# Optimization experiments

Hardware: AMD Instinct MI355X
Metric: run time of the kernel (lower is better)

Reference implementation:

```python
import jax, jax.numpy as jnp
import numpy as np

NMOL, NATOM, NPAIR = 32, 512, 32768
NBASIS, HIDDEN, NSPEC = 64, 256, 8
RC = 5.0
TOTNATOM = NMOL * NATOM


def setup_inputs() -> dict:
    key = jax.random.key(0)
    ks = jax.random.split(key, 8)
    cart = jax.random.normal(ks[0], (NMOL, NATOM, 3), jnp.float32) * 3.0
    shifts = jax.random.normal(ks[1], (NMOL, NPAIR, 3), jnp.float32) * 0.1
    species = jax.random.randint(ks[2], (NMOL, NATOM), 0, NSPEC)
    atom_index = jax.random.randint(ks[3], (2, NMOL, NPAIR), 0, NATOM)
    numatoms = jnp.full((NMOL,), NATOM, jnp.int32)
    centers = jnp.linspace(0.0, RC, NBASIS).astype(jnp.float32)
    widths = jnp.full((NBASIS,), 0.5, jnp.float32)
    c_emb = jax.random.normal(ks[4], (NSPEC, NBASIS), jnp.float32)
    W1 = jax.random.normal(ks[5], (NBASIS, HIDDEN), jnp.float32) / np.sqrt(NBASIS).astype(np.float32)
    b1 = jnp.zeros((HIDDEN,), jnp.float32)
    W2 = jax.random.normal(ks[6], (HIDDEN, 1), jnp.float32) / np.sqrt(HIDDEN).astype(np.float32)
    b2 = jnp.zeros((1,), jnp.float32)
    return dict(cart=cart, shifts=shifts, centers=centers, widths=widths, c_emb=c_emb,
                W1=W1, b1=b1, W2=W2, b2=b2,
                numatoms=numatoms, species=species, atom_index=atom_index)


def reference(cart, shifts, centers, widths, c_emb, W1, b1, W2, b2, numatoms, species, atom_index):
    species_flat = species.reshape(-1)                      # [totnatom]
    cart_flat = cart.reshape(-1, 3)                         # [totnatom, 3]
    # per-molecule atom offset, expanded over pairs (matches self_mol_index)
    mol_off = (jnp.arange(NMOL, dtype=atom_index.dtype) * NATOM)  # [nmol]
    off = jnp.broadcast_to(mol_off[:, None], (NMOL, NPAIR)).reshape(-1)  # [npairs_tot]
    idx12 = atom_index.reshape(2, -1) + off[None, :]        # [2, npairs_tot]
    shifts_flat = shifts.reshape(-1, 3)
    # padding mask (torch code drops rows with shift == -1e10; we mask instead)
    valid = jnp.all(shifts_flat > -1e10, axis=1)
    mask_f = valid.astype(cart.dtype)                       # [npairs_tot]
    # gather pair coords, periodic-shifted displacement
    c0 = cart_flat[idx12[0]]                                # [npairs_tot, 3]
    c1 = cart_flat[idx12[1]]
    dist_vec = (c0 - c1 + shifts_flat) * mask_f[:, None]    # [npairs_tot, 3]
    d = jnp.sqrt(jnp.sum(dist_vec * dist_vec, axis=1) + 1e-12)  # safe norm
    # embedded density: gaussian RBF * cosine cutoff * neighbor-species coeff
    rbf = jnp.exp(-widths[None, :] * (d[:, None] - centers[None, :]) ** 2)  # [P, nbasis]
    fc = 0.5 * (jnp.cos(jnp.pi * d / RC) + 1.0) * (d < RC).astype(cart.dtype)
    pair_feat = rbf * (fc * mask_f)[:, None] * c_emb[species_flat[idx12[1]]]
    density = jax.ops.segment_sum(pair_feat, idx12[0], num_segments=TOTNATOM)  # [totnatom, nbasis]
    # per-atom scalar output (nnmod)
    h = jax.nn.silu(density @ W1 + b1)
    output = (h @ W2 + b2).reshape(-1)                      # [totnatom]
    # scatter-add displacement vectors to center atom
    tot_vec = jax.ops.segment_sum(dist_vec, idx12[0], num_segments=TOTNATOM)  # [totnatom, 3]
    # weighted contraction ('i,ij->ij') + per-molecule sum -> dipole
    dipole = jnp.sum((output[:, None] * tot_vec).reshape(NMOL, NATOM, 3), axis=1)  # [nmol, 3]
    return dipole
```

## Files before the change

kernel.cpp:

```cpp
#include <hip/hip_runtime.h>

#define NMOL   32
#define NATOM  512
#define NPAIR  32768
#define NB     64
#define HIDDEN 256
#define TOTNATOM (NMOL * NATOM)
#define NSUB   8
#define BLKCAP4 4352
#define ABLK   4
#define NSLOT  128
#define CSLOT  64

typedef __attribute__((ext_vector_type(8))) short bf16x8;
typedef __attribute__((ext_vector_type(4))) float f32x4;

__device__ __forceinline__ unsigned short f2bf(float x) {
    unsigned u = __float_as_uint(x);
    u += 0x7FFFu + ((u >> 16) & 1u);
    return (unsigned short)(u >> 16);
}

__global__ __launch_bounds__(1024) void scatter_kernel(
    const float* __restrict__ cart, const float* __restrict__ shifts,
    const int* __restrict__ species, const int* __restrict__ atom_index,
    unsigned* __restrict__ cnt, unsigned* __restrict__ soff_g,
    float4* __restrict__ rec, float* __restrict__ dipole, int ndip)
{
    __shared__ float    s_cart[NATOM * 3];
    __shared__ int      s_sp[NATOM];
    __shared__ unsigned lcnt[NATOM];
    __shared__ unsigned pref[NATOM];
    __shared__ unsigned stot;
    __shared__ float4   list[BLKCAP4];

    const int tid  = threadIdx.x;
    const int lane = tid & 63;
    const int wave = tid >> 6;
    const int b    = blockIdx.x;
    const int mol  = b & 31;
    const int sub  = b >> 5;

    if (b == 0 && tid < ndip) dipole[tid] = 0.f;

    const float* cm = cart + (size_t)mol * NATOM * 3;
    const int*   sp = species + (size_t)mol * NATOM;
    for (int i = tid; i < NATOM * 3; i += 1024) s_cart[i] = cm[i];
    if (tid < NATOM) { lcnt[tid] = 0u; s_sp[tid] = sp[tid]; }
    __syncthreads();

    const int* ai0 = atom_index + (size_t)mol * NPAIR;
    const int* ai1 = ai0 + (size_t)NMOL * NPAIR;
    const float* sh = shifts + (size_t)mol * NPAIR * 3;
    const int base = sub * 4096;

    int   gi0[4], gi1[4];
    float gsx[4], gsy[4], gsz[4];
#pragma unroll
    for (int k = 0; k < 4; ++k) {
        const int p = base + k * 1024 + tid;
        gi0[k] = ai0[p];
        gi1[k] = ai1[p];
        gsx[k] = sh[p * 3 + 0];
        gsy[k] = sh[p * 3 + 1];
        gsz[k] = sh[p * 3 + 2];
    }

    float    rx[4], ry[4], rz[4];
    unsigned rs[4], rp[4];
    int      ri[4];
#pragma unroll
    for (int k = 0; k < 4; ++k) {
        const int a3 = gi0[k] * 3, b3 = gi1[k] * 3;
        const bool m = (gsx[k] > -1e10f && gsy[k] > -1e10f && gsz[k] > -1e10f);
        ri[k] = -1;
        if (m) {
            rx[k] = s_cart[a3 + 0] - s_cart[b3 + 0] + gsx[k];
            ry[k] = s_cart[a3 + 1] - s_cart[b3 + 1] + gsy[k];
            rz[k] = s_cart[a3 + 2] - s_cart[b3 + 2] + gsz[k];
            rs[k] = (unsigned)s_sp[gi1[k]];
            ri[k] = gi0[k];
            rp[k] = atomicAdd(&lcnt[gi0[k]], 1u);
        }
    }
    __syncthreads();

    if (wave == 0) {
        unsigned c[8], s = 0;
#pragma unroll
        for (int j = 0; j < 8; ++j) { c[j] = lcnt[lane * 8 + j]; s += c[j]; }
        unsigned incl = s;
#pragma unroll
        for (int off = 1; off < 64; off <<= 1) {
            const unsigned v = __shfl_up(incl, off);
            if (lane >= off) incl += v;
        }
        unsigned run = incl - s;
#pragma unroll
        for (int j = 0; j < 8; ++j) { pref[lane * 8 + j] = run; run += c[j]; }
        if (lane == 63) stot = incl;
    }
    __syncthreads();

#pragma unroll
    for (int k = 0; k < 4; ++k) {
        if (ri[k] >= 0) {
            const unsigned idx = pref[ri[k]] + rp[k];
            if (idx < (unsigned)BLKCAP4)
                list[idx] = make_float4(rx[k], ry[k], rz[k], __uint_as_float(rs[k]));
        }
    }
    __syncthreads();

    const int tot = min((int)stot, BLKCAP4);
    float4* dstr = rec + (size_t)b * BLKCAP4;
    for (int i = tid; i < tot; i += 1024) dstr[i] = list[i];

    if (tid < NATOM) {
        cnt[((size_t)mol * NATOM + tid) * NSUB + sub] = lcnt[tid];
        soff_g[(size_t)b * NATOM + tid] = pref[tid];
    }
}

__global__ __launch_bounds__(256) void gather_kernel(
    const unsigned* __restrict__ cnt, const unsigned* __restrict__ soff_g,
    const float4* __restrict__ rec,
    const float* __restrict__ centers, const float* __restrict__ widths,
    const float* __restrict__ c_emb,
    unsigned short* __restrict__ dens_bf, float* __restrict__ tvv)
{
    __shared__ float    cemb[8 * NB];
    __shared__ float4   list4[ABLK][NSLOT];
    __shared__ float2   cbuf[ABLK][CSLOT];
    __shared__ unsigned scnt[ABLK][NSUB];
    __shared__ unsigned sofg[ABLK][NSUB];
    __shared__ unsigned soff[ABLK][NSUB];
    __shared__ unsigned ntot[ABLK];

    const int tid   = threadIdx.x;
    const int B     = blockIdx.x;
    const int mol   = B & 31;
    const int inner = B >> 5;
    const int a0    = mol * NATOM + inner * ABLK;
    const int ra0   = inner * ABLK;

    for (int i = tid; i < 8 * NB; i += 256) cemb[i] = c_emb[i];
    if (tid < ABLK * NSUB) {
        const int al = tid >> 3, s = tid & 7;
        scnt[al][s] = cnt[(size_t)(a0 + al) * NSUB + s];
        sofg[al][s] = soff_g[(size_t)(s * NMOL + mol) * NATOM + (ra0 + al)];
    }
    __syncthreads();

    if (tid < ABLK) {
        int o = 0;
#pragma unroll
        for (int s = 0; s < NSUB; ++s) {
            soff[tid][s] = (unsigned)o;
            o += min((int)scnt[tid][s], NSLOT - o);
        }
        ntot[tid] = (unsigned)o;
    }
    __syncthreads();

    {
        const int seg = tid >> 3;
        const int prt = tid & 7;
        const int al = seg >> 3, s = seg & 7;
        const int off = (int)soff[al][s];
        const int n = min((int)scnt[al][s], NSLOT - off);
        const float4* src = rec + (size_t)(s * NMOL + mol) * BLKCAP4 + sofg[al][s];
        float4* dst = &list4[al][off];
        for (int k = prt; k < n; k += 8) dst[k] = src[k];
    }
    __syncthreads();

    const int lane = tid & 63;
    const int al   = tid >> 6;
    const int a    = a0 + al;

    const float L2E = 1.4426950408889634f;
    const float wl  = widths[lane];
    const float cl  = centers[lane];
    const float qe  = -wl * L2E;
    const float qb  = 2.f * wl * cl * L2E;
    const float qa  = -wl * cl * cl * L2E;

    const int n = (int)ntot[al];
    float tx = 0.f, ty = 0.f, tz = 0.f;
    int mbase = 0;
    for (int c0 = 0; c0 < n; c0 += 64) {
        const int k = c0 + lane;
        const bool valid = (k < n);
        float4 q = make_float4(0.f, 0.f, 0.f, 0.f);
        if (valid) q = list4[al][k];
        tx += q.x; ty += q.y; tz += q.z;
        const float d = sqrtf(q.x * q.x + q.y * q.y + q.z * q.z + 1e-12f);
        const bool in = valid && (d < 5.0f);
        const unsigned long long mask = __ballot(in);
        if (in) {
            const float fc = 0.5f * (__cosf(0.62831853071795864769f * d) + 1.f);
            const unsigned fb = (__float_as_uint(fc) & ~7u)
                              | (__float_as_uint(q.w) & 7u);
            const int pos = __builtin_amdgcn_mbcnt_hi((unsigned)(mask >> 32),
                          __builtin_amdgcn_mbcnt_lo((unsigned)mask, 0u));
            const int idx = mbase + pos;
            if (idx < CSLOT) cbuf[al][idx] = make_float2(d, __uint_as_float(fb));
        }
        mbase += (int)__popcll(mask);
    }
    if (mbase > CSLOT) mbase = CSLOT;
    const int mp = (mbase + 7) & ~7;
    if (lane < mp - mbase) cbuf[al][mbase + lane] = make_float2(0.f, 0.f);
#pragma unroll
    for (int off = 32; off; off >>= 1) {
        tx += __shfl_down(tx, off);
        ty += __shfl_down(ty, off);
        tz += __shfl_down(tz, off);
    }
    if (lane == 0) {
        tvv[(size_t)a * 3 + 0] = tx;
        tvv[(size_t)a * 3 + 1] = ty;
        tvv[(size_t)a * 3 + 2] = tz;
    }

#define REC1(A, dv, fv) { const unsigned f_ = __float_as_uint(fv);           \
        const float v_ = fmaf(dv, fmaf(dv, qe, qb), qa);                     \
        A = fmaf(exp2f(v_) * __uint_as_float(f_ & ~7u),                      \
                 cemb[((f_ & 7u) << 6) | lane], A); }
    const float4* l4 = reinterpret_cast<const float4*>(cbuf[al]);
    float acc0 = 0.f, acc1 = 0.f;
    for (int j = 0; j < mp; j += 8) {
        const float4 q0 = l4[(j >> 1) + 0];
        const float4 q1 = l4[(j >> 1) + 1];
        const float4 q2 = l4[(j >> 1) + 2];
        const float4 q3 = l4[(j >> 1) + 3];
        REC1(acc0, q0.x, q0.y) REC1(acc1, q0.z, q0.w)
        REC1(acc0, q1.x, q1.y) REC1(acc1, q1.z, q1.w)
        REC1(acc0, q2.x, q2.y) REC1(acc1, q2.z, q2.w)
        REC1(acc0, q3.x, q3.y) REC1(acc1, q3.z, q3.w)
    }
#undef REC1
    dens_bf[(size_t)a * NB + lane] = f2bf(acc0 + acc1);
}

__global__ __launch_bounds__(256) void nn_kernel(
    const unsigned short* __restrict__ dens_bf, const float* __restrict__ tvv,
    const float* __restrict__ W1, const float* __restrict__ b1,
    const float* __restrict__ W2, const float* __restrict__ b2,
    float* __restrict__ dipole)
{
    __shared__ __align__(16) unsigned short w1t[HIDDEN * 72];
    __shared__ float b1_l[HIDDEN], w2_l[HIDDEN];
    __shared__ float sred[4][4][3];

    const int tid   = threadIdx.x;
    const int B     = blockIdx.x;
    const int mol   = B & 31;
    const int chunk = B >> 5;

    for (int i = tid; i < NB * HIDDEN; i += 256) {
        const int k = i >> 8, j = i & 255;
        w1t[j * 72 + k] = f2bf(W1[i]);
    }
    if (tid < HIDDEN) { b1_l[tid] = b1[tid]; w2_l[tid] = W2[tid]; }
    __syncthreads();

    const int lane = tid & 63;
    const int wave = tid >> 6;
    const int fr   = lane & 15;
    const int fg   = lane >> 4;
    const int a0w  = mol * NATOM + chunk * 64 + wave * 16;

    bf16x8 afr[2];
#pragma unroll
    for (int kk = 0; kk < 2; ++kk)
        afr[kk] = *reinterpret_cast<const bf16x8*>(
            dens_bf + (size_t)(a0w + fr) * NB + kk * 32 + fg * 8);

    float sdip[4] = {0.f, 0.f, 0.f, 0.f};
#pragma unroll
    for (int nt = 0; nt < 16; ++nt) {
        const bf16x8 bf0 = *reinterpret_cast<const bf16x8*>(
            &w1t[(nt * 16 + fr) * 72 + 0 + fg * 8]);
        const bf16x8 bf1 = *reinterpret_cast<const bf16x8*>(
            &w1t[(nt * 16 + fr) * 72 + 32 + fg * 8]);
        f32x4 acc = {0.f, 0.f, 0.f, 0.f};
        acc = __builtin_amdgcn_mfma_f32_16x16x32_bf16(afr[0], bf0, acc, 0, 0, 0);
        acc = __builtin_amdgcn_mfma_f32_16x16x32_bf16(afr[1], bf1, acc, 0, 0, 0);
        const int j = nt * 16 + fr;
        const float b1v = b1_l[j], w2v = w2_l[j];
#pragma unroll
        for (int i = 0; i < 4; ++i) {
            const float h = acc[i] + b1v;
            sdip[i] += (h / (1.f + __expf(-h))) * w2v;
        }
    }
#pragma unroll
    for (int off = 1; off < 16; off <<= 1) {
#pragma unroll
        for (int i = 0; i < 4; ++i) sdip[i] += __shfl_xor(sdip[i], off);
    }
    if (fr == 0) {
        const float b2v = b2[0];
        float px = 0.f, py = 0.f, pz = 0.f;
#pragma unroll
        for (int i = 0; i < 4; ++i) {
            const int a = a0w + fg * 4 + i;
            const float out = sdip[i] + b2v;
            px += out * tvv[a * 3 + 0];
            py += out * tvv[a * 3 + 1];
            pz += out * tvv[a * 3 + 2];
        }
        sred[wave][fg][0] = px; sred[wave][fg][1] = py; sred[wave][fg][2] = pz;
    }
    __syncthreads();
    if (tid < 3) {
        float s = 0.f;
#pragma unroll
        for (int w = 0; w < 4; ++w)
#pragma unroll
            for (int g = 0; g < 4; ++g) s += sred[w][g][tid];
        unsafeAtomicAdd(&dipole[mol * 3 + tid], s);
    }
}

extern "C" void kernel_launch(void* const* d_in, const int* in_sizes, int n_in,
                              void* d_out, int out_size, void* d_ws, size_t ws_size,
                              hipStream_t stream)
{
    const float* cart       = (const float*)d_in[0];
    const float* shifts     = (const float*)d_in[1];
    const float* centers    = (const float*)d_in[2];
    const float* widths     = (const float*)d_in[3];
    const float* c_emb      = (const float*)d_in[4];
    const float* W1         = (const float*)d_in[5];
    const float* b1         = (const float*)d_in[6];
    const float* W2         = (const float*)d_in[7];
    const float* b2         = (const float*)d_in[8];
    const int*   species    = (const int*)d_in[10];
    const int*   atom_index = (const int*)d_in[11];

    unsigned*       cnt     = (unsigned*)d_ws;
    unsigned*       soff_g  = cnt + (size_t)TOTNATOM * NSUB;
    float*          tvv     = (float*)(soff_g + (size_t)NMOL * NSUB * NATOM);
    unsigned short* dens_bf = (unsigned short*)(tvv + (size_t)TOTNATOM * 3);
    float4*         rec     = (float4*)(dens_bf + (size_t)TOTNATOM * NB);
    float*          dipole  = (float*)d_out;

    hipLaunchKernelGGL(scatter_kernel, dim3(NMOL * NSUB), dim3(1024), 0, stream,
                       cart, shifts, species, atom_index, cnt, soff_g, rec,
                       dipole, out_size);
    hipLaunchKernelGGL(gather_kernel, dim3(TOTNATOM / ABLK), dim3(256), 0, stream,
                       cnt, soff_g, rec, centers, widths, c_emb, dens_bf, tvv);
    hipLaunchKernelGGL(nn_kernel, dim3(TOTNATOM / 64), dim3(256), 0, stream,
                       dens_bf, tvv, W1, b1, W2, b2, dipole);
}
```

Measured before the change: 42.32 us.

## Compact in-cutoff pair records in scatter kernel and precompute partial displacement sums

```diff
diff --git a/kernel.cpp b/kernel.cpp
--- a/kernel.cpp
+++ b/kernel.cpp
@@ -8,9 +8,9 @@
 #define TOTNATOM (NMOL * NATOM)
 #define NSUB   8
 #define BLKCAP4 4352
+#define BLKCAP2 2816
 #define ABLK   4
-#define NSLOT  128
-#define CSLOT  64
+#define NSLOT  48
 
 typedef __attribute__((ext_vector_type(8))) short bf16x8;
 typedef __attribute__((ext_vector_type(4))) float f32x4;
@@ -25,14 +25,18 @@
     const float* __restrict__ cart, const float* __restrict__ shifts,
     const int* __restrict__ species, const int* __restrict__ atom_index,
     unsigned* __restrict__ cnt, unsigned* __restrict__ soff_g,
-    float4* __restrict__ rec, float* __restrict__ dipole, int ndip)
+    float2* __restrict__ rec, float* __restrict__ tv_part,
+    float* __restrict__ dipole, int ndip)
 {
     __shared__ float    s_cart[NATOM * 3];
     __shared__ int      s_sp[NATOM];
     __shared__ unsigned lcnt[NATOM];
     __shared__ unsigned pref[NATOM];
-    __shared__ unsigned stot;
+    __shared__ unsigned ccnt[NATOM];
+    __shared__ unsigned pref2[NATOM];
+    __shared__ unsigned stot2;
     __shared__ float4   list[BLKCAP4];
+    __shared__ float2   out2[BLKCAP2];
 
     const int tid  = threadIdx.x;
     const int lane = tid & 63;
@@ -98,7 +102,6 @@
         unsigned run = incl - s;
 #pragma unroll
         for (int j = 0; j < 8; ++j) { pref[lane * 8 + j] = run; run += c[j]; }
-        if (lane == 63) stot = incl;
     }
     __syncthreads();
 
@@ -112,30 +115,84 @@
     }
     __syncthreads();
 
-    const int tot = min((int)stot, BLKCAP4);
-    float4* dstr = rec + (size_t)b * BLKCAP4;
-    for (int i = tid; i < tot; i += 1024) dstr[i] = list[i];
-
     if (tid < NATOM) {
-        cnt[((size_t)mol * NATOM + tid) * NSUB + sub] = lcnt[tid];
-        soff_g[(size_t)b * NATOM + tid] = pref[tid];
+        const int a  = tid;
+        const int j0 = (int)pref[a];
+        const int j1 = min(j0 + (int)lcnt[a], BLKCAP4);
+        float tx = 0.f, ty = 0.f, tz = 0.f;
+        unsigned c2 = 0;
+        for (int j = j0; j < j1; ++j) {
+            const float4 q = list[j];
+            tx += q.x; ty += q.y; tz += q.z;
+            const float d = sqrtf(q.x * q.x + q.y * q.y + q.z * q.z + 1e-12f);
+            if (d < 5.0f) ++c2;
+        }
+        ccnt[a] = c2;
+        float* tg = tv_part + ((size_t)b * NATOM + a) * 3;
+        tg[0] = tx; tg[1] = ty; tg[2] = tz;
+    }
+    __syncthreads();
+
+    if (wave == 0) {
+        unsigned c[8], s = 0;
+#pragma unroll
+        for (int j = 0; j < 8; ++j) { c[j] = ccnt[lane * 8 + j]; s += c[j]; }
+        unsigned incl = s;
+#pragma unroll
+        for (int off = 1; off < 64; off <<= 1) {
+            const unsigned v = __shfl_up(incl, off);
+            if (lane >= off) incl += v;
+        }
+        unsigned run = incl - s;
+#pragma unroll
+        for (int j = 0; j < 8; ++j) { pref2[lane * 8 + j] = run; run += c[j]; }
+        if (lane == 63) stot2 = incl;
+    }
+    __syncthreads();
+
+    if (tid < NATOM) {
+        const int a  = tid;
+        const int j0 = (int)pref[a];
+        const int j1 = min(j0 + (int)lcnt[a], BLKCAP4);
+        unsigned w = pref2[a];
+        for (int j = j0; j < j1; ++j) {
+            const float4 q = list[j];
+            const float d = sqrtf(q.x * q.x + q.y * q.y + q.z * q.z + 1e-12f);
+            if (d < 5.0f) {
+                const float fc = 0.5f * (__cosf(0.62831853071795864769f * d) + 1.f);
+                const unsigned fb = (__float_as_uint(fc) & ~7u)
+                                  | (__float_as_uint(q.w) & 7u);
+                if (w < (unsigned)BLKCAP2)
+                    out2[w] = make_float2(d, __uint_as_float(fb));
+                ++w;
+            }
+        }
+    }
+    __syncthreads();
+
+    const int tot = min((int)stot2, BLKCAP2);
+    float2* dstr = rec + (size_t)b * BLKCAP2;
+    for (int i = tid; i < tot; i += 1024) dstr[i] = out2[i];
+
+    if (tid < NATOM) {
+        cnt[((size_t)mol * NATOM + tid) * NSUB + sub] = ccnt[tid];
+        soff_g[(size_t)b * NATOM + tid] = pref2[tid];
     }
 }
 
 __global__ __launch_bounds__(256) void gather_kernel(
     const unsigned* __restrict__ cnt, const unsigned* __restrict__ soff_g,
-    const float4* __restrict__ rec,
+    const float2* __restrict__ rec,
     const float* __restrict__ centers, const float* __restrict__ widths,
-    const float* __restrict__ c_emb,
+    const float* __restrict__ c_emb, const float* __restrict__ tv_part,
     unsigned short* __restrict__ dens_bf, float* __restrict__ tvv)
 {
     __shared__ float    cemb[8 * NB];
-    __shared__ float4   list4[ABLK][NSLOT];
-    __shared__ float2   cbuf[ABLK][CSLOT];
+    __shared__ float2   list2[ABLK][NSLOT];
     __shared__ unsigned scnt[ABLK][NSUB];
     __shared__ unsigned sofg[ABLK][NSUB];
     __shared__ unsigned soff[ABLK][NSUB];
-    __shared__ unsigned ntot[ABLK];
+    __shared__ unsigned mtot[ABLK];
 
     const int tid   = threadIdx.x;
     const int B     = blockIdx.x;
@@ -159,7 +216,10 @@
             soff[tid][s] = (unsigned)o;
             o += min((int)scnt[tid][s], NSLOT - o);
         }
-        ntot[tid] = (unsigned)o;
+        const int mp = (o + 7) & ~7;
+        mtot[tid] = (unsigned)(mp <= NSLOT ? mp : NSLOT & ~7);
+        for (int k = o; k < mp && k < NSLOT; ++k)
+            list2[tid][k] = make_float2(0.f, 0.f);
     }
     __syncthreads();
 
@@ -169,9 +229,17 @@
         const int al = seg >> 3, s = seg & 7;
         const int off = (int)soff[al][s];
         const int n = min((int)scnt[al][s], NSLOT - off);
-        const float4* src = rec + (size_t)(s * NMOL + mol) * BLKCAP4 + sofg[al][s];
-        float4* dst = &list4[al][off];
+        const float2* src = rec + (size_t)(s * NMOL + mol) * BLKCAP2 + sofg[al][s];
+        float2* dst = &list2[al][off];
         for (int k = prt; k < n; k += 8) dst[k] = src[k];
+    }
+    if (tid < ABLK * 3) {
+        const int al = tid / 3, c = tid - al * 3;
+        float s = 0.f;
+#pragma unroll
+        for (int sb = 0; sb < NSUB; ++sb)
+            s += tv_part[((size_t)(sb * NMOL + mol) * NATOM + (ra0 + al)) * 3 + c];
+        tvv[(size_t)(a0 + al) * 3 + c] = s;
     }
     __syncthreads();
 
@@ -186,49 +254,12 @@
     const float qb  = 2.f * wl * cl * L2E;
     const float qa  = -wl * cl * cl * L2E;
 
-    const int n = (int)ntot[al];
-    float tx = 0.f, ty = 0.f, tz = 0.f;
-    int mbase = 0;
-    for (int c0 = 0; c0 < n; c0 += 64) {
-        const int k = c0 + lane;
-        const bool valid = (k < n);
-        float4 q = make_float4(0.f, 0.f, 0.f, 0.f);
-        if (valid) q = list4[al][k];
-        tx += q.x; ty += q.y; tz += q.z;
-        const float d = sqrtf(q.x * q.x + q.y * q.y + q.z * q.z + 1e-12f);
-        const bool in = valid && (d < 5.0f);
-        const unsigned long long mask = __ballot(in);
-        if (in) {
-            const float fc = 0.5f * (__cosf(0.62831853071795864769f * d) + 1.f);
-            const unsigned fb = (__float_as_uint(fc) & ~7u)
-                              | (__float_as_uint(q.w) & 7u);
-            const int pos = __builtin_amdgcn_mbcnt_hi((unsigned)(mask >> 32),
-                          __builtin_amdgcn_mbcnt_lo((unsigned)mask, 0u));
-            const int idx = mbase + pos;
-            if (idx < CSLOT) cbuf[al][idx] = make_float2(d, __uint_as_float(fb));
-        }
-        mbase += (int)__popcll(mask);
-    }
-    if (mbase > CSLOT) mbase = CSLOT;
-    const int mp = (mbase + 7) & ~7;
-    if (lane < mp - mbase) cbuf[al][mbase + lane] = make_float2(0.f, 0.f);
-#pragma unroll
-    for (int off = 32; off; off >>= 1) {
-        tx += __shfl_down(tx, off);
-        ty += __shfl_down(ty, off);
-        tz += __shfl_down(tz, off);
-    }
-    if (lane == 0) {
-        tvv[(size_t)a * 3 + 0] = tx;
-        tvv[(size_t)a * 3 + 1] = ty;
-        tvv[(size_t)a * 3 + 2] = tz;
-    }
-
 #define REC1(A, dv, fv) { const unsigned f_ = __float_as_uint(fv);           \
         const float v_ = fmaf(dv, fmaf(dv, qe, qb), qa);                     \
         A = fmaf(exp2f(v_) * __uint_as_float(f_ & ~7u),                      \
                  cemb[((f_ & 7u) << 6) | lane], A); }
-    const float4* l4 = reinterpret_cast<const float4*>(cbuf[al]);
+    const int mp = (int)mtot[al];
+    const float4* l4 = reinterpret_cast<const float4*>(list2[al]);
     float acc0 = 0.f, acc1 = 0.f;
     for (int j = 0; j < mp; j += 8) {
         const float4 q0 = l4[(j >> 1) + 0];
@@ -344,15 +375,17 @@
     unsigned*       cnt     = (unsigned*)d_ws;
     unsigned*       soff_g  = cnt + (size_t)TOTNATOM * NSUB;
     float*          tvv     = (float*)(soff_g + (size_t)NMOL * NSUB * NATOM);
-    unsigned short* dens_bf = (unsigned short*)(tvv + (size_t)TOTNATOM * 3);
-    float4*         rec     = (float4*)(dens_bf + (size_t)TOTNATOM * NB);
+    float*          tv_part = tvv + (size_t)TOTNATOM * 3;
+    unsigned short* dens_bf = (unsigned short*)(tv_part + (size_t)NMOL * NSUB * NATOM * 3);
+    float2*         rec     = (float2*)(dens_bf + (size_t)TOTNATOM * NB);
     float*          dipole  = (float*)d_out;
 
     hipLaunchKernelGGL(scatter_kernel, dim3(NMOL * NSUB), dim3(1024), 0, stream,
                        cart, shifts, species, atom_index, cnt, soff_g, rec,
-                       dipole, out_size);
+                       tv_part, dipole, out_size);
     hipLaunchKernelGGL(gather_kernel, dim3(TOTNATOM / ABLK), dim3(256), 0, stream,
-                       cnt, soff_g, rec, centers, widths, c_emb, dens_bf, tvv);
+                       cnt, soff_g, rec, centers, widths, c_emb, tv_part,
+                       dens_bf, tvv);
     hipLaunchKernelGGL(nn_kernel, dim3(TOTNATOM / 64), dim3(256), 0, stream,
                        dens_bf, tvv, W1, b1, W2, b2, dipole);
 }
```

Result: faster. 40.72 us (-3.8%).
